# Kernel optimization log

Hardware: AMD Instinct MI355X
Metric: run time of the kernel (lower is better)

Reference implementation:

```python
import jax, jax.numpy as jnp
import numpy as np

B, N, E = 16, 512, 131072
FEAT, EMB, H = 3, 512, 3
K1, K2 = 410, 205  # ceil(0.8*512), ceil(0.5*410) per PyG TopKPooling
NEG_SLOPE, EPS = 0.2, 1e-5


def _gat_conv(x, W, att_s, att_d, bias, src, tgt, valid, num_nodes):
    # PyG GATConv (concat=True): per-edge attention with segment softmax over targets.
    Hh, C = att_s.shape
    xp = (x @ W).reshape(-1, Hh, C)                      # [Nn,H,C]
    a_s = jnp.einsum('nhc,hc->nh', xp, att_s)
    a_d = jnp.einsum('nhc,hc->nh', xp, att_d)
    srcc = jnp.where(valid, src, 0)
    tgtc = jnp.where(valid, tgt, 0)
    e = jax.nn.leaky_relu(a_s[srcc] + a_d[tgtc], NEG_SLOPE)  # [Ee,H]
    seg = jnp.where(valid, tgt, num_nodes)               # invalid edges -> dummy segment
    emax = jax.ops.segment_max(e, seg, num_segments=num_nodes + 1)
    emax = jnp.where(jnp.isfinite(emax), emax, 0.0)
    ex = jnp.exp(e - emax[seg]) * valid[:, None].astype(e.dtype)
    den = jax.ops.segment_sum(ex, seg, num_segments=num_nodes + 1)
    alpha = ex / jnp.maximum(den[seg], 1e-16)            # [Ee,H]
    out = jax.ops.segment_sum(alpha[:, :, None] * xp[srcc], seg,
                              num_segments=num_nodes + 1)[:num_nodes]
    return out.reshape(num_nodes, Hh * C) + bias


def _bn(x, g, b):
    # BatchNorm1d, training-mode batch statistics (biased var), eps=1e-5
    m = x.mean(0)
    v = x.var(0)
    return (x - m) * jax.lax.rsqrt(v + EPS) * g + b


def _topk_pool(x, p, nb, n_per, k):
    # PyG TopKPooling: score = tanh(x.w/||w||), keep top-k per graph, scale by score
    score = jnp.tanh((x @ p) / jnp.linalg.norm(p))       # [nb*n_per]
    top_s, top_i = jax.lax.top_k(score.reshape(nb, n_per), k)
    perm = (top_i + jnp.arange(nb)[:, None] * n_per).reshape(-1)
    x_new = x[perm] * top_s.reshape(-1, 1)
    mapping = jnp.full((nb * n_per,), -1, jnp.int32).at[perm].set(
        jnp.arange(nb * k, dtype=jnp.int32))
    return x_new, mapping


def _pool_cat(x, nb, k):
    # [global_max_pool, global_mean_pool] over equal-size graphs
    xr = x.reshape(nb, k, -1)
    return jnp.concatenate([xr.max(1), xr.mean(1)], axis=1)


def _forward(x, W1, as1, ad1, bc1, Wh1, bh1, g1, be1, p1,
             W2, as2, ad2, bc2, Wh2, bh2, g2, be2, p2,
             Wl1, bl1, Wl2, bl2, edge_index):
    Nn = B * N
    src0, tgt0 = edge_index[0], edge_index[1]
    sl = jnp.arange(Nn, dtype=jnp.int32)                 # GATConv add_self_loops=True
    src1 = jnp.concatenate([src0, sl]); tgt1 = jnp.concatenate([tgt0, sl])
    valid1 = jnp.ones(src1.shape, bool)
    h = _gat_conv(x, W1, as1, ad1, bc1, src1, tgt1, valid1, Nn)
    h = jax.nn.relu(h @ Wh1 + bh1)
    h = _bn(h, g1, be1)
    h, mapping = _topk_pool(h, p1, B, N, K1)
    x1 = _pool_cat(h, B, K1)                             # [B, 2*EMB]
    # relabel edges to pooled node ids; drop edges with removed endpoints via mask
    s2 = mapping[src0]; t2 = mapping[tgt0]
    v2 = (s2 >= 0) & (t2 >= 0)
    sl2 = jnp.arange(B * K1, dtype=jnp.int32)
    src2 = jnp.concatenate([s2, sl2]); tgt2 = jnp.concatenate([t2, sl2])
    valid2 = jnp.concatenate([v2, jnp.ones(sl2.shape, bool)])
    h = _gat_conv(h, W2, as2, ad2, bc2, src2, tgt2, valid2, B * K1)
    h = jax.nn.relu(h @ Wh2 + bh2)
    h = _bn(h, g2, be2)
    h, _ = _topk_pool(h, p2, B, K1, K2)
    x2 = _pool_cat(h, B, K2)
    xg = x1 + x2
    xg = jax.nn.relu(xg @ Wl1 + bl1)                     # dropout p=0.5 disabled (eval)
    return xg @ Wl2 + bl2                                # [B, 256]


def setup_inputs() -> dict:
    key = jax.random.key(0)
    ks = jax.random.split(key, 16)
    x = jax.random.normal(ks[0], (B * N, FEAT), jnp.float32)
    goff = jnp.repeat(jnp.arange(B, dtype=jnp.int32), E // B) * N
    src = jax.random.randint(ks[1], (E,), 0, N, jnp.int32) + goff
    tgt = jax.random.randint(ks[2], (E,), 0, N, jnp.int32) + goff
    edge_index = jnp.stack([src, tgt])
    s = 0.05
    p = {
        'W1': jax.random.normal(ks[3], (FEAT, H * EMB)) * s,
        'as1': jax.random.normal(ks[4], (H, EMB)) * s,
        'ad1': jax.random.normal(ks[5], (H, EMB)) * s,
        'bc1': jnp.zeros((H * EMB,)),
        'Wh1': jax.random.normal(ks[6], (H * EMB, EMB)) * s,
        'bh1': jnp.zeros((EMB,)),
        'g1': jnp.ones((EMB,)), 'be1': jnp.zeros((EMB,)),
        'p1': jax.random.normal(ks[7], (EMB,)) * s,
        'W2': jax.random.normal(ks[8], (EMB, H * EMB)) * s,
        'as2': jax.random.normal(ks[9], (H, EMB)) * s,
        'ad2': jax.random.normal(ks[10], (H, EMB)) * s,
        'bc2': jnp.zeros((H * EMB,)),
        'Wh2': jax.random.normal(ks[11], (H * EMB, EMB)) * s,
        'bh2': jnp.zeros((EMB,)),
        'g2': jnp.ones((EMB,)), 'be2': jnp.zeros((EMB,)),
        'p2': jax.random.normal(ks[12], (EMB,)) * s,
        'Wl1': jax.random.normal(ks[13], (2 * EMB, 512)) * s,
        'bl1': jnp.zeros((512,)),
        'Wl2': jax.random.normal(ks[14], (512, 256)) * s,
        'bl2': jnp.zeros((256,)),
    }
    return {'x': x, 'edge_index': edge_index, **p}


def reference(x, edge_index, W1, as1, ad1, bc1, Wh1, bh1, g1, be1, p1,
              W2, as2, ad2, bc2, Wh2, bh2, g2, be2, p2, Wl1, bl1, Wl2, bl2):
    return _forward(x, W1, as1, ad1, bc1, Wh1, bh1, g1, be1, p1,
                    W2, as2, ad2, bc2, Wh2, bh2, g2, be2, p2,
                    Wl1, bl1, Wl2, bl2, edge_index)
```

## Files before the change

### kernel.cpp

```cpp
#include <hip/hip_runtime.h>
#include <hip/hip_bf16.h>
#include <math.h>

#define E_EDGES 131072
#define NN1 8192
#define NN2 6560
#define NG 16
#define NP1 512
#define KP1 410
#define KP2 205
#define F1 1536
#define EMB 512
#define MAXDEG 256

typedef __hip_bfloat16 bf16;
typedef __attribute__((ext_vector_type(8))) short short8;
typedef __attribute__((ext_vector_type(4))) float f32x4;
typedef __attribute__((ext_vector_type(4))) unsigned short us4;

__device__ inline float wred64(float v){
  #pragma unroll
  for (int o = 32; o; o >>= 1) v += __shfl_down(v, o);
  return v;
}
__device__ inline float b2f_raw(unsigned short u){
  return __uint_as_float((unsigned)u << 16);
}
union BFU { bf16 b; unsigned short u; };
__device__ inline unsigned short f2u(float v){ BFU x; x.b = __float2bfloat16(v); return x.u; }

__device__ __forceinline__ void gld16(const void* g, void* l){
  __builtin_amdgcn_global_load_lds(
      (const __attribute__((address_space(1))) void*)g,
      (__attribute__((address_space(3))) void*)l, 16, 0, 0);
}

__device__ inline void split_store(float v, bf16* __restrict__ ph, bf16* __restrict__ pl){
  bf16 hi = __float2bfloat16(v);
  *ph = hi;
  *pl = __float2bfloat16(v - __bfloat162float(hi));
}

__device__ inline void bn_from_acc(const float* __restrict__ bnacc, int c, float fM,
                                   float& mean, float& inv){
  mean = bnacc[c] / fM;
  float var = fmaxf(bnacc[512+c]/fM - mean*mean, 0.f);
  inv = 1.f / sqrtf(var + 1e-5f);
}

__global__ __launch_bounds__(256) void k_pre(
    const float* __restrict__ W1, const float* __restrict__ as1, const float* __restrict__ ad1,
    const float* __restrict__ Wh1, const float* __restrict__ bc1, const float* __restrict__ bh1,
    const float* __restrict__ W2, const float* __restrict__ as2, const float* __restrict__ ad2,
    const float* __restrict__ Wh2, const float* __restrict__ bc2, const float* __restrict__ bh2,
    float* __restrict__ was1, float* __restrict__ wad1, float* __restrict__ M1p,
    float* __restrict__ cvp,
    float* __restrict__ was2, float* __restrict__ wad2,
    float* __restrict__ Zb, int* __restrict__ cnt2, int* __restrict__ map,
    bf16* __restrict__ Th, bf16* __restrict__ Tl){
  int b = blockIdx.x, t = threadIdx.x;
  if (b < 24){
    int h = b / 8, rem = b % 8, jh = rem >> 2, kc = rem & 3;
    int j = jh*256 + t, c0 = kc*128;
    __shared__ float w1s[3][128];
    for (int i = t; i < 384; i += 256)
      w1s[i>>7][i&127] = W1[(i>>7)*1536 + h*512 + c0 + (i&127)];
    __syncthreads();
    const float* whc = Wh1 + (size_t)(h*512 + c0)*512 + j;
    float a0=0.f, a1=0.f, a2=0.f;
    #pragma unroll 8
    for (int c = 0; c < 128; c++){
      float v = whc[(size_t)c*512];
      a0 += w1s[0][c]*v; a1 += w1s[1][c]*v; a2 += w1s[2][c]*v;
    }
    float* dst = M1p + (size_t)kc*4608;
    dst[(h*3+0)*512 + j] = a0;
    dst[(h*3+1)*512 + j] = a1;
    dst[(h*3+2)*512 + j] = a2;
  } else if (b < 56){
    int b2 = b - 24;
    int which = b2 >> 4, rem = b2 & 15, jh = rem >> 3, kc = rem & 7;
    const float* bc = which ? bc2 : bc1;
    const float* Wh = which ? Wh2 : Wh1;
    const float* bh = which ? bh2 : bh1;
    int j = jh*256 + t, i0 = kc*192;
    float acc = (kc == 0) ? bh[j] : 0.f;
    #pragma unroll 8
    for (int i = 0; i < 192; i++)
      acc += bc[i0+i] * Wh[(size_t)(i0+i)*512 + j];
    cvp[(size_t)(which*8 + kc)*512 + j] = acc;
  } else if (b < 152){
    int b3 = b - 56;
    int y = b3 >> 4, et = b3 & 15;
    int kind = y / 3, h = y % 3;
    int w = t >> 6, lane = t & 63;
    const float* att = kind ? ad2 : as2;
    float a[8];
    #pragma unroll
    for (int u = 0; u < 8; u++) a[u] = att[h*512 + lane*8 + u];
    for (int r = w; r < 32; r += 4){
      int e = et*32 + r;
      const float4* row = (const float4*)(W2 + (size_t)e*1536 + h*512) + lane*2;
      float4 v0 = row[0], v1 = row[1];
      float d = v0.x*a[0]+v0.y*a[1]+v0.z*a[2]+v0.w*a[3]
              + v1.x*a[4]+v1.y*a[5]+v1.z*a[6]+v1.w*a[7];
      d = wred64(d);
      if (lane == 0) (kind ? wad2 : was2)[h*512 + e] = d;
    }
  } else if (b < 170){
    if (t < 64){
      int bb = b - 152;
      int kind = bb / 9, r = bb % 9, h = r / 3, f = r % 3;
      const float* att = kind ? ad1 : as1;
      float s = 0.f;
      for (int c = t; c < 512; c += 64) s += W1[f*1536 + h*512 + c] * att[h*512 + c];
      s = wred64(s);
      if (t == 0) (kind ? wad1 : was1)[h*3 + f] = s;
    }
  } else if (b < 236){
    int i = (b - 170)*256 + t;
    if (i < 2048){ Zb[i] = 0.f; }
    else if (i < 2048 + NN2){ cnt2[i - 2048] = 1; }
    else if (i < 2048 + NN2 + NN1){ map[i - 2048 - NN2] = -1; }
  } else {
    int bb = b - 236;
    int z = bb % 3; int rr = bb / 3; int by = rr >> 3, bx = rr & 7;
    const float* A = W2 + (size_t)z*512;
    const float* B = Wh2 + (size_t)z*512*512;
    __shared__ __align__(16) short sAh[4096], sAl[4096], sBh[4096], sBl[4096];
    int w = t >> 6, lane = t & 63;
    int l16 = lane & 15, q = lane >> 4;
    int bm = by*64, bn = bx*64;
    int am  = t >> 2, akw = (t & 3)*16;
    int bnl = t & 63, bkq = (t >> 6)*16;
    f32x4 acc[4];
    #pragma unroll
    for (int nf = 0; nf < 4; nf++) acc[nf] = (f32x4){0.f,0.f,0.f,0.f};
    float va[16], vb[16];
    #define GS_LOAD(K0) do { \
      _Pragma("unroll") for (int u = 0; u < 4; u++){ \
        float4 v4 = *(const float4*)(A + (size_t)(bm+am)*1536 + (K0) + akw + u*4); \
        va[u*4]=v4.x; va[u*4+1]=v4.y; va[u*4+2]=v4.z; va[u*4+3]=v4.w; } \
      _Pragma("unroll") for (int u = 0; u < 16; u++) \
        vb[u] = B[(size_t)((K0) + bkq + u)*512 + bn + bnl]; \
    } while(0)
    GS_LOAD(0);
    for (int it = 0; it < 8; it++){
      #pragma unroll
      for (int hh = 0; hh < 2; hh++){
        short8 ah_, al_, bh_, bl_;
        #pragma unroll
        for (int jj = 0; jj < 8; jj++){
          float v = va[hh*8+jj];
          unsigned short hu = f2u(v);
          ah_[jj] = (short)hu; al_[jj] = (short)f2u(v - b2f_raw(hu));
          v = vb[hh*8+jj];
          hu = f2u(v);
          bh_[jj] = (short)hu; bl_[jj] = (short)f2u(v - b2f_raw(hu));
        }
        int aoff = am*64  + ((((akw>>3) + hh) ^ (am  & 7)) << 3);
        *(short8*)(sAh + aoff) = ah_;
        *(short8*)(sAl + aoff) = al_;
        int boff = bnl*64 + ((((bkq>>3) + hh) ^ (bnl & 7)) << 3);
        *(short8*)(sBh + boff) = bh_;
        *(short8*)(sBl + boff) = bl_;
      }
      __syncthreads();
      if (it < 7) GS_LOAD((it+1)*64);
      #pragma unroll
      for (int ks = 0; ks < 2; ks++){
        int gc = ks*4 + q;
        int ar = w*16 + l16;
        int ao = ar*64 + ((gc ^ (ar & 7)) << 3);
        short8 afh = *(const short8*)(sAh + ao);
        short8 afl = *(const short8*)(sAl + ao);
        #pragma unroll
        for (int nf = 0; nf < 4; nf++){
          int br = nf*16 + l16;
          int bo = br*64 + ((gc ^ (br & 7)) << 3);
          short8 bfh = *(const short8*)(sBh + bo);
          short8 bfl = *(const short8*)(sBl + bo);
          acc[nf] = __builtin_amdgcn_mfma_f32_16x16x32_bf16(afh, bfh, acc[nf], 0, 0, 0);
          acc[nf] = __builtin_amdgcn_mfma_f32_16x16x32_bf16(afh, bfl, acc[nf], 0, 0, 0);
          acc[nf] = __builtin_amdgcn_mfma_f32_16x16x32_bf16(afl, bfh, acc[nf], 0, 0, 0);
        }
      }
      __syncthreads();
    }
    #undef GS_LOAD
    int m0 = bm + w*16 + q*4;
    #pragma unroll
    for (int nf = 0; nf < 4; nf++){
      int n = bn + nf*16 + l16;
      size_t base = (size_t)n*1536 + (size_t)z*512 + m0;
      #pragma unroll
      for (int e = 0; e < 4; e++)
        split_store(acc[nf][e], &Th[base+e], &Tl[base+e]);
    }
  }
}

__global__ __launch_bounds__(256) void k_edge(
    const int* __restrict__ src0, const int* __restrict__ tgt0, const float* __restrict__ x,
    const float* __restrict__ was, const float* __restrict__ wad,
    float* __restrict__ denp, float* __restrict__ nump){
  int b = blockIdx.x, t = threadIdx.x;
  int g = b >> 4, ch = b & 15;
  __shared__ float lden[1536];
  __shared__ float lnum[4608];
  for (int i = t; i < 1536; i += 256) lden[i] = 0.f;
  for (int i = t; i < 4608; i += 256) lnum[i] = 0.f;
  __syncthreads();
  int base = g*8192;
  int it0 = ch*544;
  for (int k = t; k < 544; k += 256){
    int it = it0 + k;
    int s, tl;
    if (it < 8192){ s = src0[base+it]; tl = tgt0[base+it] & 511; }
    else { tl = it - 8192; s = g*512 + tl; }
    float xs0 = x[s*3], xs1 = x[s*3+1], xs2 = x[s*3+2];
    int tg = g*512 + tl;
    float xt0 = x[tg*3], xt1 = x[tg*3+1], xt2 = x[tg*3+2];
    #pragma unroll
    for (int h = 0; h < 3; h++){
      float v = xs0*was[h*3]+xs1*was[h*3+1]+xs2*was[h*3+2]
              + xt0*wad[h*3]+xt1*wad[h*3+1]+xt2*wad[h*3+2];
      v = v > 0.f ? v : 0.2f*v;
      float pe = expf(v);
      atomicAdd(&lden[tl*3 + h], pe);
      atomicAdd(&lnum[tl*9 + h*3 + 0], pe * xs0);
      atomicAdd(&lnum[tl*9 + h*3 + 1], pe * xs1);
      atomicAdd(&lnum[tl*9 + h*3 + 2], pe * xs2);
    }
  }
  __syncthreads();
  for (int i = t; i < 4608; i += 256) nump[(size_t)b*4608 + i] = lnum[i];
  for (int i = t; i < 1536; i += 256) denp[(size_t)b*1536 + i] = lden[i];
}

__global__ __launch_bounds__(256) void k_h1(
    const float* __restrict__ nump, const float* __restrict__ denp,
    const float* __restrict__ M1p, const float* __restrict__ cvp1, bf16* __restrict__ hout,
    float* __restrict__ bnacc1){
  __shared__ float sM[9*512];
  __shared__ float sC[512];
  __shared__ float sA[32*9];
  int t = threadIdx.x; int n0 = blockIdx.x*32;
  for (int i = t; i < 9*512; i += 256)
    sM[i] = M1p[i] + M1p[4608 + i] + M1p[2*4608 + i] + M1p[3*4608 + i];
  for (int i = t; i < 512; i += 256){
    float s = 0.f;
    #pragma unroll
    for (int kc = 0; kc < 8; kc++) s += cvp1[kc*512 + i];
    sC[i] = s;
  }
  for (int i = t; i < 288; i += 256){
    int node = i / 9, q = i % 9, hh = q / 3;
    int gn = n0 + node;
    int g = gn >> 9, nl = gn & 511;
    float ns = 0.f, ds = 0.f;
    #pragma unroll 4
    for (int ch = 0; ch < 16; ch++){
      ns += nump[(size_t)(g*16 + ch)*4608 + nl*9 + q];
      ds += denp[(size_t)(g*16 + ch)*1536 + nl*3 + hh];
    }
    sA[i] = ns / fmaxf(ds, 1e-16f);
  }
  __syncthreads();
  float c0v = sC[t], c1v = sC[t+256];
  float ls0=0.f, lq0=0.f, ls1=0.f, lq1=0.f;
  #pragma unroll 4
  for (int i = 0; i < 32; i++){
    float a0 = c0v, a1 = c1v;
    #pragma unroll
    for (int q = 0; q < 9; q++){
      float av = sA[i*9+q];
      a0 += av * sM[q*512 + t];
      a1 += av * sM[q*512 + t + 256];
    }
    a0 = fmaxf(a0, 0.f); a1 = fmaxf(a1, 0.f);
    hout[(size_t)(n0+i)*512 + t]       = __float2bfloat16(a0);
    hout[(size_t)(n0+i)*512 + t + 256] = __float2bfloat16(a1);
    ls0 += a0; lq0 += a0*a0; ls1 += a1; lq1 += a1*a1;
  }
  atomicAdd(&bnacc1[t],           ls0);
  atomicAdd(&bnacc1[t+256],       ls1);
  atomicAdd(&bnacc1[512 + t],     lq0);
  atomicAdd(&bnacc1[512 + t+256], lq1);
}

__global__ __launch_bounds__(512) void k_scoresort(
    const bf16* __restrict__ h, const float* __restrict__ bnacc, int M,
    const float* __restrict__ g_, const float* __restrict__ be, const float* __restrict__ p,
    int n_per, int K, int* __restrict__ map,
    int* __restrict__ topi, float* __restrict__ tops){
  int g = blockIdx.x, t = threadIdx.x;
  __shared__ float w[512];
  __shared__ float redb[8], redp[8];
  __shared__ float sk[512];
  __shared__ int si[512];
  float fM = (float)M;
  float mean, inv; bn_from_acc(bnacc, t, fM, mean, inv);
  float gc = g_[t], pc = p[t];
  float ig = inv * gc;
  w[t] = ig * pc;
  float bt = (be[t] - mean * ig) * pc;
  float b_ = wred64(bt);
  float pp = wred64(pc * pc);
  int lane = t & 63, wv = t >> 6;
  if (lane == 0){ redb[wv] = b_; redp[wv] = pp; }
  __syncthreads();
  float B0 = 0.f, pn2 = 0.f;
  #pragma unroll
  for (int u = 0; u < 8; u++){ B0 += redb[u]; pn2 += redp[u]; }
  float pn = sqrtf(pn2);
  float score = -INFINITY; int idx = 0x7fffffff;
  if (t < n_per){
    const unsigned short* hr = (const unsigned short*)h + (size_t)(g*n_per + t)*EMB;
    float dot = 0.f;
    #pragma unroll 4
    for (int c = 0; c < 512; c += 8){
      us4 v0 = *(const us4*)(hr + c);
      us4 v1 = *(const us4*)(hr + c + 4);
      dot += b2f_raw(v0.x)*w[c]   + b2f_raw(v0.y)*w[c+1]
           + b2f_raw(v0.z)*w[c+2] + b2f_raw(v0.w)*w[c+3]
           + b2f_raw(v1.x)*w[c+4] + b2f_raw(v1.y)*w[c+5]
           + b2f_raw(v1.z)*w[c+6] + b2f_raw(v1.w)*w[c+7];
    }
    score = tanhf((dot + B0) / pn);
    idx = t;
  }
  sk[t] = score; si[t] = idx;
  __syncthreads();
  for (int k = 2; k <= 512; k <<= 1){
    for (int j = k >> 1; j > 0; j >>= 1){
      int l = t ^ j;
      if (l > t){
        float ki = sk[t], kl = sk[l]; int ii = si[t], il = si[l];
        bool before_l = (kl > ki) || (kl == ki && il < ii);
        bool up = ((t & k) == 0);
        if (up == before_l){ sk[t]=kl; sk[l]=ki; si[t]=il; si[l]=ii; }
      }
      __syncthreads();
    }
  }
  if (t < K){
    if (map) map[g*n_per + si[t]] = g*K + t;
    topi[g*K + t] = si[t];
    tops[g*K + t] = sk[t];
  }
}

__global__ __launch_bounds__(256) void k_gather_c2(
    const bf16* __restrict__ h, const float* __restrict__ bnacc, int M,
    const float* __restrict__ gm, const float* __restrict__ be,
    const int* __restrict__ topi, const float* __restrict__ tops,
    bf16* __restrict__ xn, int n_per, int K,
    const float* __restrict__ was2, const float* __restrict__ wad2,
    float* __restrict__ aso, float* __restrict__ ado,
    const int* __restrict__ src0, const int* __restrict__ tgt0,
    const int* __restrict__ map, int* __restrict__ cnt2, int nblk_g){
  int row = blockIdx.x, t = threadIdx.x;
  if (row >= nblk_g){
    int i = (row - nblk_g)*256 + t;
    if (i < E_EDGES){
      int s = map[src0[i]], tg = map[tgt0[i]];
      if (s >= 0 && tg >= 0) atomicAdd(&cnt2[tg], 1);
    }
    return;
  }
  int gr = row / K, i = row - gr*K;
  int sidx = topi[gr*K + i];
  float s = tops[gr*K + i];
  const bf16* src = h + ((size_t)(gr*n_per + sidx))*EMB;
  bf16* dst = xn + (size_t)row*EMB;
  int c0 = t, c1 = t + 256;
  float fM = (float)M;
  float mean0, inv0, mean1, inv1;
  bn_from_acc(bnacc, c0, fM, mean0, inv0);
  bn_from_acc(bnacc, c1, fM, mean1, inv1);
  float v0 = ((__bfloat162float(src[c0]) - mean0) * inv0 * gm[c0] + be[c0]) * s;
  float v1 = ((__bfloat162float(src[c1]) - mean1) * inv1 * gm[c1] + be[c1]) * s;
  dst[c0] = __float2bfloat16(v0);
  dst[c1] = __float2bfloat16(v1);
  {
    float a[6];
    #pragma unroll
    for (int hh = 0; hh < 3; hh++){
      a[hh]   = v0*was2[hh*512 + c0] + v1*was2[hh*512 + c1];
      a[3+hh] = v0*wad2[hh*512 + c0] + v1*wad2[hh*512 + c1];
    }
    __shared__ float red[6][4];
    int lane = t & 63, wv = t >> 6;
    #pragma unroll
    for (int q = 0; q < 6; q++){ float v = wred64(a[q]); if (lane==0) red[q][wv]=v; }
    __syncthreads();
    if (t < 6){
      float sm = red[t][0]+red[t][1]+red[t][2]+red[t][3];
      if (t < 3) aso[row*3+t] = sm; else ado[row*3+(t-3)] = sm;
    }
  }
}

__device__ inline void scan_body(const int* __restrict__ counts, int* __restrict__ off,
                                 int* __restrict__ cur, int n, int* __restrict__ sh){
  int t = threadIdx.x;
  int chunk = (n + 1023) >> 10;
  int b = t * chunk; int e = b + chunk; if (e > n) e = n;
  int s = 0;
  for (int i = b; i < e; i++) s += counts[i];
  sh[t] = s; __syncthreads();
  for (int o = 1; o < 1024; o <<= 1){
    int v = (t >= o) ? sh[t-o] : 0;
    __syncthreads();
    sh[t] += v;
    __syncthreads();
  }
  int run = (t > 0) ? sh[t-1] : 0;
  for (int i = b; i < e; i++){ int c = counts[i]; off[i] = run; cur[i] = run; run += c; }
  if (t == 1023) off[n] = sh[1023];
}
__global__ void k_fill2(const int* __restrict__ src0, const int* __restrict__ tgt0,
                        const int* __restrict__ map, int* __restrict__ cur,
                        int* __restrict__ esrc, int E, int nn){
  int i = blockIdx.x*blockDim.x + threadIdx.x;
  if (i >= E + nn) return;
  int s, tg;
  if (i < E){
    s = map[src0[i]]; tg = map[tgt0[i]];
    if (s < 0 || tg < 0) return;
  } else { s = i - E; tg = s; }
  int pos = atomicAdd(&cur[tg], 1);
  esrc[pos] = s;
}

__global__ __launch_bounds__(1024) void k_poolA_scan(const bf16* __restrict__ xn,
    float* __restrict__ cat, int K,
    const int* __restrict__ cnt2, int* __restrict__ off2, int* __restrict__ cur2){
  __shared__ int shi[1024];
  __shared__ float smax[8][128];
  __shared__ float ssum[8][128];
  int b = blockIdx.x, t = threadIdx.x;
  if (b == 64){ scan_body(cnt2, off2, cur2, NN2, shi); return; }
  int g = b >> 2, cb = b & 3;
  int c = t & 127, rg = t >> 7;
  int col = cb*128 + c;
  const unsigned short* p = (const unsigned short*)xn + (size_t)g*K*EMB + col;
  float mx = -INFINITY, sm = 0.f;
  for (int r = rg; r < K; r += 8){
    float v = b2f_raw(p[(size_t)r*EMB]);
    mx = fmaxf(mx, v); sm += v;
  }
  smax[rg][c] = mx; ssum[rg][c] = sm;
  __syncthreads();
  if (rg == 0){
    #pragma unroll
    for (int u = 1; u < 8; u++){ mx = fmaxf(mx, smax[u][c]); sm += ssum[u][c]; }
    cat[g*1024 + col] = mx;
    cat[g*1024 + 512 + col] = sm / (float)K;
  }
}
__global__ __launch_bounds__(1024) void k_poolB(const bf16* __restrict__ h,
    const float* __restrict__ bnacc, int M,
    const float* __restrict__ gm, const float* __restrict__ be,
    const int* __restrict__ topi, const float* __restrict__ tops,
    float* __restrict__ cat, int n_per, int K){
  __shared__ int sti[256];
  __shared__ float sts[256];
  __shared__ float smax[8][128];
  __shared__ float ssum[8][128];
  int b = blockIdx.x, t = threadIdx.x;
  int g = b >> 2, cb = b & 3;
  for (int r = t; r < K; r += 1024){ sti[r] = topi[g*K + r]; sts[r] = tops[g*K + r]; }
  __syncthreads();
  int c = t & 127, rg = t >> 7;
  int col = cb*128 + c;
  float fM = (float)M;
  float mean, inv; bn_from_acc(bnacc, col, fM, mean, inv);
  float gg = gm[col], bb = be[col];
  const unsigned short* hp = (const unsigned short*)h;
  float mx = -INFINITY, sm = 0.f;
  for (int r = rg; r < K; r += 8){
    float v = (b2f_raw(hp[(size_t)(g*n_per + sti[r])*EMB + col]) - mean) * inv * gg + bb;
    v *= sts[r];
    mx = fmaxf(mx, v); sm += v;
  }
  smax[rg][c] = mx; ssum[rg][c] = sm;
  __syncthreads();
  if (rg == 0){
    #pragma unroll
    for (int u = 1; u < 8; u++){ mx = fmaxf(mx, smax[u][c]); sm += ssum[u][c]; }
    cat[g*1024 + col] = mx;
    cat[g*1024 + 512 + col] = sm / (float)K;
  }
}

__global__ __launch_bounds__(256) void k_agg2(
    const bf16* __restrict__ xn, const float* __restrict__ aso, const float* __restrict__ ado,
    const int* __restrict__ off, const int* __restrict__ esrc,
    bf16* __restrict__ oh){
  int n = blockIdx.x, t = threadIdx.x;
  __shared__ int srcs[MAXDEG];
  __shared__ float al[MAXDEG*3];
  __shared__ float mh[3], dh[3];
  int s0 = off[n]; int deg = off[n+1] - s0; if (deg > MAXDEG) deg = MAXDEG;
  for (int e = t; e < deg; e += 256) srcs[e] = esrc[s0 + e];
  __syncthreads();
  float ad0 = ado[n*3+0], ad1 = ado[n*3+1], ad2 = ado[n*3+2];
  for (int e = t; e < deg; e += 256){
    int s = srcs[e];
    float v0 = aso[s*3+0] + ad0, v1 = aso[s*3+1] + ad1, v2 = aso[s*3+2] + ad2;
    al[e*3+0] = v0 > 0.f ? v0 : 0.2f*v0;
    al[e*3+1] = v1 > 0.f ? v1 : 0.2f*v1;
    al[e*3+2] = v2 > 0.f ? v2 : 0.2f*v2;
  }
  __syncthreads();
  if (t < 3){
    float m = -INFINITY;
    for (int e = 0; e < deg; e++) m = fmaxf(m, al[e*3+t]);
    float d = 0.f;
    for (int e = 0; e < deg; e++) d += expf(al[e*3+t] - m);
    mh[t] = m; dh[t] = 1.f / fmaxf(d, 1e-16f);
  }
  __syncthreads();
  for (int e = t; e < deg; e += 256){
    al[e*3+0] = expf(al[e*3+0]-mh[0])*dh[0];
    al[e*3+1] = expf(al[e*3+1]-mh[1])*dh[1];
    al[e*3+2] = expf(al[e*3+2]-mh[2])*dh[2];
  }
  __syncthreads();
  float acc[2][3] = {};
  for (int e = 0; e < deg; e++){
    int s = srcs[e];
    float a0 = al[e*3], a1 = al[e*3+1], a2 = al[e*3+2];
    #pragma unroll
    for (int k = 0; k < 2; k++){
      float v = __bfloat162float(xn[(size_t)s*512 + t + k*256]);
      acc[k][0] += a0*v; acc[k][1] += a1*v; acc[k][2] += a2*v;
    }
  }
  #pragma unroll
  for (int k = 0; k < 2; k++){
    int c = t + k*256;
    #pragma unroll
    for (int h = 0; h < 3; h++)
      oh[(size_t)n*1536 + h*512 + c] = __float2bfloat16(acc[k][h]);
  }
}

__global__ __launch_bounds__(256, 2) void k_gemm_mfma(
    const bf16* __restrict__ Ah,
    const bf16* __restrict__ Bh, const bf16* __restrict__ Bl,
    const float* __restrict__ bias, bf16* __restrict__ C,
    float* __restrict__ bnacc,
    int M, int N, int K, int Mtiles){
  int xcd = (int)blockIdx.x & 7;
  int ii  = (int)blockIdx.x >> 3;
  int bni = ii & 7;
  int bmi = xcd + 8*(ii >> 3);
  if (bmi >= Mtiles) return;
  __shared__ __align__(16) unsigned short lds[2][16384];
  int t = threadIdx.x, w = t >> 6, lane = t & 63;
  int q = lane >> 4, l16 = lane & 15;
  int bm = bmi * 128, bn = bni * 64;

  int lr = lane >> 3, lc = lane & 7;
  int kg = ((lc ^ lr) & 7) * 8;
  int ro = w*8 + lr;
  int m0 = bm + ro, m1 = bm + 32 + ro, m2 = bm + 64 + ro, m3 = bm + 96 + ro;
  if (m0 >= M) m0 = M-1;  if (m1 >= M) m1 = M-1;
  if (m2 >= M) m2 = M-1;  if (m3 >= M) m3 = M-1;
  int n0 = bn + ro, n1 = bn + 32 + ro;
  const bf16* ptr[8];
  ptr[0] = Ah + (size_t)m0*K + kg;
  ptr[1] = Ah + (size_t)m1*K + kg;
  ptr[2] = Ah + (size_t)m2*K + kg;
  ptr[3] = Ah + (size_t)m3*K + kg;
  ptr[4] = Bh + (size_t)n0*K + kg;
  ptr[5] = Bh + (size_t)n1*K + kg;
  ptr[6] = Bl + (size_t)n0*K + kg;
  ptr[7] = Bl + (size_t)n1*K + kg;
  const int dof[8] = {0, 2048, 4096, 6144, 8192, 10240, 12288, 14336};

  int wm = (w >> 1) * 64, wn = (w & 1) * 32;
  f32x4 acc[4][2];
  #pragma unroll
  for (int i = 0; i < 4; i++)
    #pragma unroll
    for (int j = 0; j < 2; j++)
      acc[i][j] = (f32x4){0.f, 0.f, 0.f, 0.f};

  #pragma unroll
  for (int u = 0; u < 8; u++){
    gld16(ptr[u], &lds[0][dof[u] + w*512]);
    ptr[u] += 64;
  }

  int nit = K >> 6;
  for (int it = 0; it < nit; it++){
    __syncthreads();
    int cur = it & 1;
    if (it + 1 < nit){
      int nxt = cur ^ 1;
      #pragma unroll
      for (int u = 0; u < 8; u++){
        gld16(ptr[u], &lds[nxt][dof[u] + w*512]);
        ptr[u] += 64;
      }
    }
    const unsigned short* L = lds[cur];
    #pragma unroll
    for (int ks = 0; ks < 2; ks++){
      short8 ah[4], bh2[2], bl2[2];
      int gc = ks*4 + q;
      #pragma unroll
      for (int i = 0; i < 4; i++){
        int r = wm + i*16 + l16;
        ah[i] = *(const short8*)(L + r*64 + ((gc ^ (r & 7)) << 3));
      }
      #pragma unroll
      for (int j = 0; j < 2; j++){
        int r = wn + j*16 + l16;
        int so = ((gc ^ (r & 7)) << 3);
        bh2[j] = *(const short8*)(L + 8192  + r*64 + so);
        bl2[j] = *(const short8*)(L + 12288 + r*64 + so);
      }
      #pragma unroll
      for (int i = 0; i < 4; i++)
        #pragma unroll
        for (int j = 0; j < 2; j++){
          acc[i][j] = __builtin_amdgcn_mfma_f32_16x16x32_bf16(ah[i], bh2[j], acc[i][j], 0, 0, 0);
          acc[i][j] = __builtin_amdgcn_mfma_f32_16x16x32_bf16(ah[i], bl2[j], acc[i][j], 0, 0, 0);
        }
    }
  }

  __syncthreads();
  float* cs = (float*)&lds[0][0];
  float* cq = cs + 128;
  int slot = w >> 1;
  #pragma unroll
  for (int j = 0; j < 2; j++){
    int c_local = wn + j*16 + l16;
    int c = bn + c_local;
    float bv = 0.f;
    if (bias){
      #pragma unroll
      for (int kc = 0; kc < 8; kc++) bv += bias[kc*512 + c];
    }
    float ls = 0.f, lq = 0.f;
    #pragma unroll
    for (int i = 0; i < 4; i++){
      int rb = bm + wm + i*16 + q*4;
      #pragma unroll
      for (int e = 0; e < 4; e++){
        int r = rb + e;
        if (r < M){
          float v = fmaxf(acc[i][j][e] + bv, 0.f);
          C[(size_t)r*N + c] = __float2bfloat16(v);
          ls += v; lq += v*v;
        }
      }
    }
    ls += __shfl_xor(ls, 16); ls += __shfl_xor(ls, 32);
    lq += __shfl_xor(lq, 16); lq += __shfl_xor(lq, 32);
    if (q == 0){ cs[slot*64 + c_local] = ls; cq[slot*64 + c_local] = lq; }
  }
  __syncthreads();
  if (t < 64){
    atomicAdd(&bnacc[bn + t],        cs[t] + cs[64 + t]);
    atomicAdd(&bnacc[512 + bn + t],  cq[t] + cq[64 + t]);
  }
}

__global__ __launch_bounds__(1024) void k_head(const float* __restrict__ c1,
    const float* __restrict__ c2, const float* __restrict__ Wl1,
    const float* __restrict__ bl1, const float* __restrict__ Wl2,
    const float* __restrict__ bl2, float* __restrict__ out){
  int g = blockIdx.x, t = threadIdx.x;
  __shared__ float xg[1024];
  __shared__ float t1[512];
  __shared__ float part[2][512];
  xg[t] = c1[g*1024 + t] + c2[g*1024 + t];
  __syncthreads();
  int c = t & 511, kc = t >> 9;
  float acc = 0.f;
  #pragma unroll 8
  for (int k = kc*512; k < kc*512 + 512; k++)
    acc += xg[k] * Wl1[(size_t)k*512 + c];
  part[kc][c] = acc;
  __syncthreads();
  if (kc == 0) t1[c] = fmaxf(part[0][c] + part[1][c] + bl1[c], 0.f);
  __syncthreads();
  if (t < 512){
    int c2i = t & 255, k2 = t >> 8;
    float a = 0.f;
    #pragma unroll 8
    for (int k = k2*256; k < k2*256 + 256; k++)
      a += t1[k] * Wl2[(size_t)k*256 + c2i];
    part[k2][c2i] = a;
  }
  __syncthreads();
  if (t < 256)
    out[g*256 + t] = part[0][t] + part[1][t] + bl2[t];
}

extern "C" void kernel_launch(void* const* d_in, const int* in_sizes, int n_in,
                              void* d_out, int out_size, void* d_ws, size_t ws_size,
                              hipStream_t stream){
  const float* x   = (const float*)d_in[0];
  const int*   ei  = (const int*)d_in[1];
  const float* W1  = (const float*)d_in[2];
  const float* as1 = (const float*)d_in[3];
  const float* ad1 = (const float*)d_in[4];
  const float* bc1 = (const float*)d_in[5];
  const float* Wh1 = (const float*)d_in[6];
  const float* bh1 = (const float*)d_in[7];
  const float* g1  = (const float*)d_in[8];
  const float* be1 = (const float*)d_in[9];
  const float* p1  = (const float*)d_in[10];
  const float* W2  = (const float*)d_in[11];
  const float* as2 = (const float*)d_in[12];
  const float* ad2 = (const float*)d_in[13];
  const float* bc2 = (const float*)d_in[14];
  const float* Wh2 = (const float*)d_in[15];
  const float* bh2 = (const float*)d_in[16];
  const float* g2  = (const float*)d_in[17];
  const float* be2 = (const float*)d_in[18];
  const float* p2  = (const float*)d_in[19];
  const float* Wl1 = (const float*)d_in[20];
  const float* bl1 = (const float*)d_in[21];
  const float* Wl2 = (const float*)d_in[22];
  const float* bl2 = (const float*)d_in[23];
  float* out = (float*)d_out;

  const int* src0 = ei;
  const int* tgt0 = ei + E_EDGES;

  bf16* Cc      = (bf16*)d_ws;
  bf16* xn1     = Cc + (size_t)NN1*EMB;
  bf16* aggx2h  = xn1 + (size_t)NN2*EMB;
  bf16* M2Th    = aggx2h + (size_t)NN2*F1;
  bf16* M2Tl    = M2Th + (size_t)EMB*F1;
  float* holeA  = (float*)(M2Tl + (size_t)EMB*F1);
  float* bnacc1 = holeA + 122880;
  float* bnacc  = bnacc1 + 1024;
  float* M1p    = bnacc + 1024;
  float* cvp    = M1p + 4*4608;
  float* was2   = cvp + 16*512;
  float* wad2   = was2 + 3*512;
  float* was1   = wad2 + 3*512;
  float* wad1   = was1 + 16;
  float* aso2   = wad1 + 16;
  float* ado2   = aso2 + (size_t)NN2*3;
  float* tops   = ado2 + (size_t)NN2*3;
  float* cat1   = tops + NG*KP1;
  float* cat2   = cat1 + NG*1024;
  int* topi     = (int*)(cat2 + NG*1024);
  int* map      = topi + NG*KP1;
  int* cnt2     = map + NN1;
  int* off2     = cnt2 + NN2;
  int* cur2     = off2 + NN2 + 8;
  int* esrc2    = cur2 + NN2;
  float* nump   = (float*)(esrc2 + 137700);
  float* denp   = nump + (size_t)256*4608;
  float* cvp2   = cvp + 8*512;

  k_pre<<<428,256,0,stream>>>(W1,as1,ad1,Wh1,bc1,bh1, W2,as2,ad2,Wh2,bc2,bh2,
                              was1,wad1,M1p,cvp,was2,wad2,
                              bnacc1,cnt2,map,M2Th,M2Tl);
  k_edge<<<256,256,0,stream>>>(src0,tgt0,x,was1,wad1,denp,nump);
  k_h1<<<NN1/32,256,0,stream>>>(nump,denp,M1p,cvp,Cc,bnacc1);
  k_scoresort<<<NG,512,0,stream>>>(Cc,bnacc1,NN1,g1,be1,p1,NP1,KP1,map,topi,tops);
  k_gather_c2<<<NG*KP1+512,256,0,stream>>>(Cc,bnacc1,NN1,g1,be1,topi,tops,xn1,NP1,KP1,
      was2,wad2,aso2,ado2, src0,tgt0,map,cnt2,NG*KP1);
  k_poolA_scan<<<65,1024,0,stream>>>(xn1,cat1,KP1, cnt2,off2,cur2);
  k_fill2<<<(E_EDGES+NN2+255)/256,256,0,stream>>>(src0,tgt0,map,cur2,esrc2,E_EDGES,NN2);
  k_agg2<<<NN2,256,0,stream>>>(xn1,aso2,ado2,off2,esrc2,aggx2h);
  k_gemm_mfma<<<448,256,0,stream>>>(aggx2h,M2Th,M2Tl,cvp2,Cc,bnacc,NN2,EMB,F1,52);
  k_scoresort<<<NG,512,0,stream>>>(Cc,bnacc,NN2,g2,be2,p2,KP1,KP2,(int*)nullptr,topi,tops);
  k_poolB<<<64,1024,0,stream>>>(Cc,bnacc,NN2,g2,be2,topi,tops,cat2,KP1,KP2);
  k_head<<<NG,1024,0,stream>>>(cat1,cat2,Wl1,bl1,Wl2,bl2,out);
}
```

Before: 330.4 us.

## Split MLP head into tiled first-layer GEMM and per-graph second layer

Replaces the single 16-block head kernel with two kernels. The first spreads the 1024x512 first linear layer over 64 blocks, each staging a 128x64 Wl1 tile and all 16 graph inputs in shared memory, so every Wl1 element is read once instead of once per graph. It writes partial sums over 8 K-chunks to a scratch region in the existing workspace. A second 16-block kernel reduces those partials, applies bias and ReLU, and runs the second layer. This trades an extra launch and a small partial-sum round trip for far less redundant weight traffic and more parallelism.

```diff
diff --git a/kernel.cpp b/kernel.cpp
--- a/kernel.cpp
+++ b/kernel.cpp
@@ -673,36 +673,56 @@
   }
 }
 
-__global__ __launch_bounds__(1024) void k_head(const float* __restrict__ c1,
+__global__ __launch_bounds__(256) void k_head1p(const float* __restrict__ c1,
     const float* __restrict__ c2, const float* __restrict__ Wl1,
+    float* __restrict__ t1p){
+  __shared__ float wl[128][64];
+  __shared__ float xgs[16][128];
+  int b = blockIdx.x, t = threadIdx.x;
+  int jt = b >> 3, kc = b & 7;
+  int j0 = jt*64, k0 = kc*128;
+  for (int i = t; i < 8192; i += 256){
+    int k = i >> 6, j = i & 63;
+    wl[k][j] = Wl1[(size_t)(k0 + k)*512 + j0 + j];
+  }
+  for (int i = t; i < 2048; i += 256){
+    int g = i >> 7, k = i & 127;
+    int idx = g*1024 + k0 + k;
+    xgs[g][k] = c1[idx] + c2[idx];
+  }
+  __syncthreads();
+  #pragma unroll
+  for (int u = 0; u < 4; u++){
+    int p = t + u*256;
+    int g = p >> 6, j = p & 63;
+    float acc = 0.f;
+    #pragma unroll 8
+    for (int k = 0; k < 128; k++)
+      acc += xgs[g][k] * wl[k][j];
+    t1p[(size_t)(kc*16 + g)*512 + j0 + j] = acc;
+  }
+}
+__global__ __launch_bounds__(512) void k_head2p(const float* __restrict__ t1p,
     const float* __restrict__ bl1, const float* __restrict__ Wl2,
     const float* __restrict__ bl2, float* __restrict__ out){
+  __shared__ float t1s[512];
+  __shared__ float part[2][256];
   int g = blockIdx.x, t = threadIdx.x;
-  __shared__ float xg[1024];
-  __shared__ float t1[512];
-  __shared__ float part[2][512];
-  xg[t] = c1[g*1024 + t] + c2[g*1024 + t];
-  __syncthreads();
-  int c = t & 511, kc = t >> 9;
-  float acc = 0.f;
+  float acc = bl1[t];
+  #pragma unroll
+  for (int kc = 0; kc < 8; kc++)
+    acc += t1p[(size_t)(kc*16 + g)*512 + t];
+  t1s[t] = fmaxf(acc, 0.f);
+  __syncthreads();
+  int c = t & 255, half = t >> 8;
+  float a = 0.f;
   #pragma unroll 8
-  for (int k = kc*512; k < kc*512 + 512; k++)
-    acc += xg[k] * Wl1[(size_t)k*512 + c];
-  part[kc][c] = acc;
-  __syncthreads();
-  if (kc == 0) t1[c] = fmaxf(part[0][c] + part[1][c] + bl1[c], 0.f);
-  __syncthreads();
-  if (t < 512){
-    int c2i = t & 255, k2 = t >> 8;
-    float a = 0.f;
-    #pragma unroll 8
-    for (int k = k2*256; k < k2*256 + 256; k++)
-      a += t1[k] * Wl2[(size_t)k*256 + c2i];
-    part[k2][c2i] = a;
-  }
-  __syncthreads();
-  if (t < 256)
-    out[g*256 + t] = part[0][t] + part[1][t] + bl2[t];
+  for (int k = half*256; k < half*256 + 256; k++)
+    a += t1s[k] * Wl2[(size_t)k*256 + c];
+  part[half][c] = a;
+  __syncthreads();
+  if (half == 0)
+    out[g*256 + c] = part[0][c] + part[1][c] + bl2[c];
 }
 
 extern "C" void kernel_launch(void* const* d_in, const int* in_sizes, int n_in,
@@ -743,6 +763,7 @@
   bf16* M2Th    = aggx2h + (size_t)NN2*F1;
   bf16* M2Tl    = M2Th + (size_t)EMB*F1;
   float* holeA  = (float*)(M2Tl + (size_t)EMB*F1);
+  float* t1p    = holeA;
   float* bnacc1 = holeA + 122880;
   float* bnacc  = bnacc1 + 1024;
   float* M1p    = bnacc + 1024;
@@ -780,5 +801,6 @@
   k_gemm_mfma<<<448,256,0,stream>>>(aggx2h,M2Th,M2Tl,cvp2,Cc,bnacc,NN2,EMB,F1,52);
   k_scoresort<<<NG,512,0,stream>>>(Cc,bnacc,NN2,g2,be2,p2,KP1,KP2,(int*)nullptr,topi,tops);
   k_poolB<<<64,1024,0,stream>>>(Cc,bnacc,NN2,g2,be2,topi,tops,cat2,KP1,KP2);
-  k_head<<<NG,1024,0,stream>>>(cat1,cat2,Wl1,bl1,Wl2,bl2,out);
-}
+  k_head1p<<<64,256,0,stream>>>(cat1,cat2,Wl1,t1p);
+  k_head2p<<<NG,512,0,stream>>>(t1p,bl1,Wl2,bl2,out);
+}
```

Measured after the change: 314.2 us. 4.9% less time.
